# Optimization experiments

Measured on AMD Instinct MI355X. Metric: run time of the kernel, lower is better.

## Reference

```python
import jax, jax.numpy as jnp
import numpy as np

D_MODEL = 4096
D_FF = 11008

def setup_inputs() -> dict:
    key = jax.random.key(0)
    k1, k2, k3, k4 = jax.random.split(key, 4)
    x = jax.random.normal(k1, (2, 2048, D_MODEL), dtype=jnp.float32)
    # Linear weights stored torch-style as [out_features, in_features]
    W_gate = jax.random.normal(k2, (D_FF, D_MODEL), dtype=jnp.float32) * (D_MODEL ** -0.5)
    W_up = jax.random.normal(k3, (D_FF, D_MODEL), dtype=jnp.float32) * (D_MODEL ** -0.5)
    W_down = jax.random.normal(k4, (D_MODEL, D_FF), dtype=jnp.float32) * (D_FF ** -0.5)
    return {"x": x, "W_gate": W_gate, "W_up": W_up, "W_down": W_down}

def reference(x, W_gate, W_up, W_down):
    out_shape = x.shape[:-1] + (W_down.shape[0],)
    xf = x.reshape(-1, x.shape[-1])                      # [T, d_model]
    up = jnp.einsum('td,fd->tf', xf, W_up)               # [T, d_ff]
    gate = jax.nn.silu(jnp.einsum('td,fd->tf', xf, W_gate))  # fused SiLU on gate proj
    h = gate * up                                        # [T, d_ff]
    y = jnp.einsum('tf,df->td', h, W_down)               # [T, d_model]
    return y.reshape(out_shape)
```

## Files before the change

kernel.cpp:

```cpp
#include <hip/hip_runtime.h>
#include <hip/hip_bf16.h>

#define D_MODEL 4096
#define D_FF    11008
#define NTOK    4096

typedef __attribute__((ext_vector_type(8))) short short8;
typedef __attribute__((ext_vector_type(4))) float f32x4;

__global__ void k_cvt(const float* __restrict__ in, __hip_bfloat16* __restrict__ out, int n8) {
    int i = blockIdx.x * blockDim.x + threadIdx.x;
    if (i >= n8) return;
    const float4* p = (const float4*)in;
    float4 v0 = p[(size_t)i * 2];
    float4 v1 = p[(size_t)i * 2 + 1];
    float vals[8] = {v0.x, v0.y, v0.z, v0.w, v1.x, v1.y, v1.z, v1.w};
    short8 o;
#pragma unroll
    for (int j = 0; j < 8; ++j) {
        __hip_bfloat16 b = __float2bfloat16(vals[j]);
        o[j] = *reinterpret_cast<short*>(&b);
    }
    *reinterpret_cast<short8*>(out + (size_t)i * 8) = o;
}

static __device__ __forceinline__ void stage_half(
    const __hip_bfloat16* g, int ld, __hip_bfloat16* lds, int tid)
{
#pragma unroll
    for (int s = 0; s < 2; ++s) {
        int ci = s * 512 + tid;
        int r  = ci >> 3;
        int c  = (ci & 7) ^ (r & 7);
        __builtin_amdgcn_global_load_lds(
            (const __attribute__((address_space(1))) void*)(g + (long)r * ld + c * 8),
            (__attribute__((address_space(3))) void*)(lds + ci * 8),
            16, 0, 0);
    }
}
static __device__ __forceinline__ int sw_off(int row, int kb) {
    return row * 64 + ((((kb >> 3) ^ (row & 7))) << 3);
}

#define MFMA16(a, b, c) __builtin_amdgcn_mfma_f32_16x16x32_bf16(a, b, c, 0, 0, 0)
#define VM4D do { if (pf) asm volatile("s_waitcnt vmcnt(4)" ::: "memory");     \
                  else    asm volatile("s_waitcnt vmcnt(0)" ::: "memory"); } while (0)

#define FPHASE(cA, cB, IQ, LOADB, STAGE, VMC)                                  \
    {                                                                          \
        short8 af[2][2];                                                       \
        _Pragma("unroll")                                                      \
        for (int ii = 0; ii < 2; ++ii)                                         \
            _Pragma("unroll")                                                  \
            for (int kk = 0; kk < 2; ++kk)                                     \
                af[ii][kk] = *reinterpret_cast<const short8*>(                 \
                    &(cA)[sw_off(wm * 128 + ((IQ) * 2 + ii) * 16 + r16,        \
                                 kk * 32 + g4 * 8)]);                          \
        if (LOADB) {                                                           \
            _Pragma("unroll")                                                  \
            for (int kk = 0; kk < 2; ++kk)                                     \
                _Pragma("unroll")                                              \
                for (int j = 0; j < 2; ++j) {                                  \
                    bg[kk][j] = *reinterpret_cast<const short8*>(              \
                        &(cB)[sw_off(wn * 32 + j * 16 + r16,                   \
                                     kk * 32 + g4 * 8)]);                      \
                    bu[kk][j] = *reinterpret_cast<const short8*>(              \
                        &(cB)[8192 + sw_off(wn * 32 + j * 16 + r16,            \
                                            kk * 32 + g4 * 8)]);               \
                }                                                              \
        }                                                                      \
        STAGE;                                                                 \
        VMC;                                                                   \
        if (LOADB) asm volatile("s_waitcnt lgkmcnt(8)" ::: "memory");          \
        __builtin_amdgcn_s_barrier();                                          \
        asm volatile("s_waitcnt lgkmcnt(0)" ::: "memory");                     \
        __builtin_amdgcn_sched_barrier(0);                                     \
        __builtin_amdgcn_s_setprio(1);                                         \
        _Pragma("unroll")                                                      \
        for (int ii = 0; ii < 2; ++ii)                                         \
            _Pragma("unroll")                                                  \
            for (int j = 0; j < 2; ++j) {                                      \
                accg[(IQ) * 2 + ii][j] = MFMA16(af[ii][0], bg[0][j],           \
                                                accg[(IQ) * 2 + ii][j]);       \
                accg[(IQ) * 2 + ii][j] = MFMA16(af[ii][1], bg[1][j],           \
                                                accg[(IQ) * 2 + ii][j]);       \
                accu[(IQ) * 2 + ii][j] = MFMA16(af[ii][0], bu[0][j],           \
                                                accu[(IQ) * 2 + ii][j]);       \
                accu[(IQ) * 2 + ii][j] = MFMA16(af[ii][1], bu[1][j],           \
                                                accu[(IQ) * 2 + ii][j]);       \
            }                                                                  \
        __builtin_amdgcn_s_setprio(0);                                         \
        __builtin_amdgcn_sched_barrier(0);                                     \
        __builtin_amdgcn_s_barrier();                                          \
    }

__global__ __launch_bounds__(512, 2)
void k_gateup(const __hip_bfloat16* __restrict__ X,
              const __hip_bfloat16* __restrict__ Wg,
              const __hip_bfloat16* __restrict__ Wu,
              __hip_bfloat16* __restrict__ H,
              const float* __restrict__ Wd32,
              __hip_bfloat16* __restrict__ Wdb)
{
    extern __shared__ __hip_bfloat16 smem[];
    __hip_bfloat16* sA = smem;
    __hip_bfloat16* sB = smem + 32768;

    const int tid = threadIdx.x;
    const int bid = blockIdx.x;

    if (bid >= 1376) {
        const long total8 = (long)D_MODEL * D_FF / 8;
        const long stride = 160L * 512;
        for (long i = (long)(bid - 1376) * 512 + tid; i < total8; i += stride) {
            const float4* p = (const float4*)(Wd32 + i * 8);
            float4 v0 = p[0], v1 = p[1];
            float vals[8] = {v0.x, v0.y, v0.z, v0.w, v1.x, v1.y, v1.z, v1.w};
            short8 oo;
#pragma unroll
            for (int j = 0; j < 8; ++j) {
                __hip_bfloat16 b = __float2bfloat16(vals[j]);
                oo[j] = *reinterpret_cast<short*>(&b);
            }
            *reinterpret_cast<short8*>(Wdb + i * 8) = oo;
        }
        return;
    }

    const int lane = tid & 63;
    const int wid  = tid >> 6;
    const int wm = wid >> 2, wn = wid & 3;
    const int r16 = lane & 15, g4 = lane >> 4;

    const int xcd = bid & 7;
    const int o   = bid >> 3;
    const int n0 = (o >> 1) * 128;
    const int m0 = (xcd * 2 + (o & 1)) * 256;

    const int K = D_MODEL;
    const __hip_bfloat16* Ab = X  + (long)m0 * K;
    const __hip_bfloat16* Gb = Wg + (long)n0 * K;
    const __hip_bfloat16* Ub = Wu + (long)n0 * K;
    const long h1 = (long)128 * K;

    stage_half(Ab,        K, sA + 0,             tid);
    stage_half(Ab + h1,   K, sA + 8192,          tid);
    stage_half(Gb,        K, sB + 0,             tid);
    stage_half(Ub,        K, sB + 8192,          tid);
    stage_half(Gb + 64,   K, sB + 16384,         tid);
    stage_half(Ub + 64,   K, sB + 16384 + 8192,  tid);
    asm volatile("s_waitcnt vmcnt(4)" ::: "memory");
    __builtin_amdgcn_s_barrier();

    f32x4 accg[8][2], accu[8][2];
#pragma unroll
    for (int i = 0; i < 8; ++i)
#pragma unroll
        for (int j = 0; j < 2; ++j) {
            accg[i][j] = (f32x4){0.f, 0.f, 0.f, 0.f};
            accu[i][j] = (f32x4){0.f, 0.f, 0.f, 0.f};
        }

    const int nk = D_MODEL >> 6;
    const int niter = nk >> 1;

    for (int it = 0; it < niter; ++it) {
        const bool pf = (it + 1 < niter);
        const long ko  = (long)(2 * it + 1) * 64;
        const long kn2 = (long)(2 * it + 2) * 64;
        const long kn3 = (long)(2 * it + 3) * 64;
        short8 bg[2][2], bu[2][2];
        {
            const __hip_bfloat16* cA = sA;
            const __hip_bfloat16* cB = sB;
            FPHASE(cA, cB, 0, 1,
                stage_half(Ab + ko,      K, sA + 16384,        tid), );
            FPHASE(cA, cB, 1, 0,
                stage_half(Ab + h1 + ko, K, sA + 16384 + 8192, tid), );
            FPHASE(cA, cB, 2, 0,
                if (pf) stage_half(Gb + kn2, K, sB + 0,    tid), );
            FPHASE(cA, cB, 3, 0,
                if (pf) stage_half(Ub + kn2, K, sB + 8192, tid), VM4D);
        }
        {
            const __hip_bfloat16* cA = sA + 16384;
            const __hip_bfloat16* cB = sB + 16384;
            FPHASE(cA, cB, 0, 1,
                if (pf) stage_half(Ab + kn2,      K, sA + 0,    tid), );
            FPHASE(cA, cB, 1, 0,
                if (pf) stage_half(Ab + h1 + kn2, K, sA + 8192, tid), );
            FPHASE(cA, cB, 2, 0,
                if (pf) stage_half(Gb + kn3, K, sB + 16384,        tid), );
            FPHASE(cA, cB, 3, 0,
                if (pf) stage_half(Ub + kn3, K, sB + 16384 + 8192, tid), VM4D);
        }
    }

#pragma unroll
    for (int i = 0; i < 8; ++i)
#pragma unroll
        for (int j = 0; j < 2; ++j)
#pragma unroll
            for (int r = 0; r < 4; ++r) {
                long row = m0 + wm * 128 + i * 16 + g4 * 4 + r;
                long col = n0 + wn * 32 + j * 16 + r16;
                float g = accg[i][j][r];
                float u = accu[i][j][r];
                float s = g / (1.f + __expf(-g));
                H[row * D_FF + col] = __float2bfloat16(s * u);
            }
}

#define DPHASE(cA, cB, IQ, LOADB, STAGE, VMC)                                  \
    {                                                                          \
        short8 af[2][2];                                                       \
        _Pragma("unroll")                                                      \
        for (int ii = 0; ii < 2; ++ii)                                         \
            _Pragma("unroll")                                                  \
            for (int kk = 0; kk < 2; ++kk)                                     \
                af[ii][kk] = *reinterpret_cast<const short8*>(                 \
                    &(cA)[sw_off(wm * 128 + ((IQ) * 2 + ii) * 16 + r16,        \
                                 kk * 32 + g4 * 8)]);                          \
        if (LOADB) {                                                           \
            _Pragma("unroll")                                                  \
            for (int kk = 0; kk < 2; ++kk)                                     \
                _Pragma("unroll")                                              \
                for (int j = 0; j < 4; ++j)                                    \
                    bfr[kk][j] = *reinterpret_cast<const short8*>(             \
                        &(cB)[sw_off(wn * 64 + j * 16 + r16,                   \
                                     kk * 32 + g4 * 8)]);                      \
        }                                                                      \
        STAGE;                                                                 \
        VMC;                                                                   \
        if (LOADB) asm volatile("s_waitcnt lgkmcnt(8)" ::: "memory");          \
        __builtin_amdgcn_s_barrier();                                          \
        asm volatile("s_waitcnt lgkmcnt(0)" ::: "memory");                     \
        __builtin_amdgcn_sched_barrier(0);                                     \
        __builtin_amdgcn_s_setprio(1);                                         \
        _Pragma("unroll")                                                      \
        for (int ii = 0; ii < 2; ++ii)                                         \
            _Pragma("unroll")                                                  \
            for (int j = 0; j < 4; ++j) {                                      \
                acc[(IQ) * 2 + ii][j] = MFMA16(af[ii][0], bfr[0][j],           \
                                               acc[(IQ) * 2 + ii][j]);         \
                acc[(IQ) * 2 + ii][j] = MFMA16(af[ii][1], bfr[1][j],           \
                                               acc[(IQ) * 2 + ii][j]);         \
            }                                                                  \
        __builtin_amdgcn_s_setprio(0);                                         \
        __builtin_amdgcn_sched_barrier(0);                                     \
        __builtin_amdgcn_s_barrier();                                          \
    }

__global__ __launch_bounds__(512, 2)
void k_down(const __hip_bfloat16* __restrict__ A,
            const __hip_bfloat16* __restrict__ B,
            float* __restrict__ Y)
{
    extern __shared__ __hip_bfloat16 smem[];
    __hip_bfloat16* sA = smem;
    __hip_bfloat16* sB = smem + 32768;

    const int tid  = threadIdx.x;
    const int lane = tid & 63;
    const int wid  = tid >> 6;
    const int wm = wid >> 2, wn = wid & 3;
    const int r16 = lane & 15, g4 = lane >> 4;

    const int bid = blockIdx.x;
    const int o = (bid & 7) * 32 + (bid >> 3);
    const int n0 = (o >> 4) << 8;
    const int m0 = (o & 15) << 8;

    const int K = D_FF;
    const int N = D_MODEL;
    const __hip_bfloat16* Ab = A + (long)m0 * K;
    const __hip_bfloat16* Bb = B + (long)n0 * K;
    const long h1 = (long)128 * K;

    stage_half(Ab,            K, sA + 0,             tid);
    stage_half(Ab + h1,       K, sA + 8192,          tid);
    stage_half(Bb,            K, sB + 0,             tid);
    stage_half(Bb + h1,       K, sB + 8192,          tid);
    stage_half(Bb + 64,       K, sB + 16384,         tid);
    stage_half(Bb + h1 + 64,  K, sB + 16384 + 8192,  tid);
    asm volatile("s_waitcnt vmcnt(4)" ::: "memory");
    __builtin_amdgcn_s_barrier();

    f32x4 acc[8][4];
#pragma unroll
    for (int i = 0; i < 8; ++i)
#pragma unroll
        for (int j = 0; j < 4; ++j)
            acc[i][j] = (f32x4){0.f, 0.f, 0.f, 0.f};

    const int nk = K >> 6;
    const int niter = nk >> 1;

    for (int it = 0; it < niter; ++it) {
        const bool pf = (it + 1 < niter);
        const long ko  = (long)(2 * it + 1) * 64;
        const long kn2 = (long)(2 * it + 2) * 64;
        const long kn3 = (long)(2 * it + 3) * 64;
        {
            const __hip_bfloat16* cA = sA;
            const __hip_bfloat16* cB = sB;
            short8 bfr[2][4];
            DPHASE(cA, cB, 0, 1,
                stage_half(Ab + ko,      K, sA + 16384,        tid), );
            DPHASE(cA, cB, 1, 0,
                stage_half(Ab + h1 + ko, K, sA + 16384 + 8192, tid), );
            DPHASE(cA, cB, 2, 0,
                if (pf) stage_half(Bb + kn2,      K, sB + 0,    tid), );
            DPHASE(cA, cB, 3, 0,
                if (pf) stage_half(Bb + h1 + kn2, K, sB + 8192, tid), VM4D);
        }
        {
            const __hip_bfloat16* cA = sA + 16384;
            const __hip_bfloat16* cB = sB + 16384;
            short8 bfr[2][4];
            DPHASE(cA, cB, 0, 1,
                if (pf) stage_half(Ab + kn2,      K, sA + 0,    tid), );
            DPHASE(cA, cB, 1, 0,
                if (pf) stage_half(Ab + h1 + kn2, K, sA + 8192, tid), );
            DPHASE(cA, cB, 2, 0,
                if (pf) stage_half(Bb + kn3,      K, sB + 16384, tid), );
            DPHASE(cA, cB, 3, 0,
                if (pf) stage_half(Bb + h1 + kn3, K, sB + 16384 + 8192, tid), VM4D);
        }
    }

#pragma unroll
    for (int i = 0; i < 8; ++i)
#pragma unroll
        for (int j = 0; j < 4; ++j)
#pragma unroll
            for (int r = 0; r < 4; ++r) {
                long row = m0 + wm * 128 + i * 16 + g4 * 4 + r;
                long col = n0 + wn * 64 + j * 16 + r16;
                Y[row * N + col] = acc[i][j][r];
            }
}

extern "C" void kernel_launch(void* const* d_in, const int* in_sizes, int n_in,
                              void* d_out, int out_size, void* d_ws, size_t ws_size,
                              hipStream_t stream) {
    const float* x  = (const float*)d_in[0];
    const float* wg = (const float*)d_in[1];
    const float* wu = (const float*)d_in[2];
    const float* wd = (const float*)d_in[3];
    float* y = (float*)d_out;

    char* ws = (char*)d_ws;
    const size_t szX = (size_t)NTOK * D_MODEL * 2;
    const size_t szW = (size_t)D_FF * D_MODEL * 2;
    __hip_bfloat16* Xb  = (__hip_bfloat16*)(ws);
    __hip_bfloat16* Wgb = (__hip_bfloat16*)(ws + szX);
    __hip_bfloat16* Wub = (__hip_bfloat16*)(ws + szX + szW);
    __hip_bfloat16* Wdb = (__hip_bfloat16*)(ws + szX + 2 * szW);
    __hip_bfloat16* Hb  = (__hip_bfloat16*)(ws + szX + 3 * szW);
    (void)ws_size; (void)out_size; (void)n_in; (void)in_sizes;

    const int SMEM = 131072;
    hipFuncSetAttribute((const void*)k_gateup, hipFuncAttributeMaxDynamicSharedMemorySize, SMEM);
    hipFuncSetAttribute((const void*)k_down,   hipFuncAttributeMaxDynamicSharedMemorySize, SMEM);

    const int nX = NTOK * D_MODEL / 8;
    const int nW = D_FF * D_MODEL / 8;
    k_cvt<<<(nX + 255) / 256, 256, 0, stream>>>(x, Xb, nX);
    k_cvt<<<(nW + 255) / 256, 256, 0, stream>>>(wg, Wgb, nW);
    k_cvt<<<(nW + 255) / 256, 256, 0, stream>>>(wu, Wub, nW);

    k_gateup<<<1536, 512, SMEM, stream>>>(Xb, Wgb, Wub, Hb, wd, Wdb);
    k_down<<<256, 512, SMEM, stream>>>(Hb, Wdb, y);
}
```

Baseline: 1.004 ms.

## Fuse fp32-to-bf16 weight conversion into gate/up GEMM staging

Drops the two separate conversion kernels for W_gate and W_up. The gate/up GEMM now loads fp32 weights into registers, converts them to bf16 and writes them to LDS inside the pipelined main loop, and the block-to-tile mapping is reworked. This removes the extra write and read of the bf16 weight copies. In exchange each block re-reads fp32 weights (twice the bytes per tile, repeated across the 16 M-tiles), uses more registers, and adds a synchronous register-to-LDS path in place of the asynchronous global_load_lds.

```diff
diff --git a/kernel.cpp b/kernel.cpp
--- a/kernel.cpp
+++ b/kernel.cpp
@@ -42,7 +42,34 @@
     return row * 64 + ((((kb >> 3) ^ (row & 7))) << 3);
 }
 
+#define LOADW32(w0, w1, src)                                                   \
+    _Pragma("unroll")                                                          \
+    for (int s = 0; s < 2; ++s) {                                              \
+        int ci = s * 512 + tid;                                                \
+        int rr = ci >> 3, cc = (ci & 7) ^ (rr & 7);                            \
+        const f32x4* gp = reinterpret_cast<const f32x4*>(                      \
+            (src) + (long)rr * 4096 + cc * 8);                                 \
+        w0[s] = gp[0]; w1[s] = gp[1];                                          \
+    }
+
+#define WRITEW32(w0, w1, ldsbase)                                              \
+    _Pragma("unroll")                                                          \
+    for (int s = 0; s < 2; ++s) {                                              \
+        int ci = s * 512 + tid;                                                \
+        short8 pk;                                                             \
+        _Pragma("unroll")                                                      \
+        for (int e = 0; e < 4; ++e) {                                          \
+            __hip_bfloat16 b0 = __float2bfloat16(w0[s][e]);                    \
+            __hip_bfloat16 b1 = __float2bfloat16(w1[s][e]);                    \
+            pk[e]     = *reinterpret_cast<short*>(&b0);                        \
+            pk[4 + e] = *reinterpret_cast<short*>(&b1);                        \
+        }                                                                      \
+        *reinterpret_cast<short8*>((ldsbase) + ci * 8) = pk;                   \
+    }
+
 #define MFMA16(a, b, c) __builtin_amdgcn_mfma_f32_16x16x32_bf16(a, b, c, 0, 0, 0)
+#define VM8 asm volatile("s_waitcnt vmcnt(8)" ::: "memory")
+#define VM0 asm volatile("s_waitcnt vmcnt(0)" ::: "memory")
 #define VM4D do { if (pf) asm volatile("s_waitcnt vmcnt(4)" ::: "memory");     \
                   else    asm volatile("s_waitcnt vmcnt(0)" ::: "memory"); } while (0)
 
@@ -94,10 +121,29 @@
         __builtin_amdgcn_s_barrier();                                          \
     }
 
+#define GUTILE(XB, PF1, PF2, kA, kW)                                           \
+    {                                                                          \
+        const __hip_bfloat16* cA = sA + (XB) * 16384;                          \
+        const __hip_bfloat16* cB = sB + (XB) * 16384;                          \
+        __hip_bfloat16* nA = sA + ((XB) ^ 1) * 16384;                          \
+        __hip_bfloat16* wB = sB + (XB) * 16384;                                \
+        FPHASE(cA, cB, 0, 1,                                                   \
+            if (PF1) { stage_half(Ab + (kA),      4096, nA,        tid);       \
+                       stage_half(Ab + h1 + (kA), 4096, nA + 8192, tid); }, ); \
+        FPHASE(cA, cB, 1, 0,                                                   \
+            if (PF2) { LOADW32(wg0, wg1, G32 + (kW))                           \
+                       LOADW32(wu0, wu1, U32 + (kW)) }, );                     \
+        FPHASE(cA, cB, 2, 0, , VM8);                                           \
+        FPHASE(cA, cB, 3, 0,                                                   \
+            { VM0;                                                             \
+              if (PF2) { WRITEW32(wg0, wg1, wB)                                \
+                         WRITEW32(wu0, wu1, wB + 8192) } }, );                 \
+    }
+
 __global__ __launch_bounds__(512, 2)
 void k_gateup(const __hip_bfloat16* __restrict__ X,
-              const __hip_bfloat16* __restrict__ Wg,
-              const __hip_bfloat16* __restrict__ Wu,
+              const float* __restrict__ Wg,
+              const float* __restrict__ Wu,
               __hip_bfloat16* __restrict__ H,
               const float* __restrict__ Wd32,
               __hip_bfloat16* __restrict__ Wdb)
@@ -132,24 +178,30 @@
     const int wm = wid >> 2, wn = wid & 3;
     const int r16 = lane & 15, g4 = lane >> 4;
 
-    const int xcd = bid & 7;
-    const int o   = bid >> 3;
-    const int n0 = (o >> 1) * 128;
-    const int m0 = (xcd * 2 + (o & 1)) * 256;
-
-    const int K = D_MODEL;
-    const __hip_bfloat16* Ab = X  + (long)m0 * K;
-    const __hip_bfloat16* Gb = Wg + (long)n0 * K;
-    const __hip_bfloat16* Ub = Wu + (long)n0 * K;
-    const long h1 = (long)128 * K;
-
-    stage_half(Ab,        K, sA + 0,             tid);
-    stage_half(Ab + h1,   K, sA + 8192,          tid);
-    stage_half(Gb,        K, sB + 0,             tid);
-    stage_half(Ub,        K, sB + 8192,          tid);
-    stage_half(Gb + 64,   K, sB + 16384,         tid);
-    stage_half(Ub + 64,   K, sB + 16384 + 8192,  tid);
-    asm volatile("s_waitcnt vmcnt(4)" ::: "memory");
+    const int o = (bid & 7) * 172 + (bid >> 3);
+    const int n0 = (o >> 4) * 128;
+    const int m0 = (o & 15) * 256;
+
+    const __hip_bfloat16* Ab = X + (long)m0 * 4096;
+    const float* G32 = Wg + (long)n0 * 4096;
+    const float* U32 = Wu + (long)n0 * 4096;
+    const long h1 = (long)128 * 4096;
+
+    f32x4 wg0[2], wg1[2], wu0[2], wu1[2];
+
+    stage_half(Ab,      4096, sA + 0,    tid);
+    stage_half(Ab + h1, 4096, sA + 8192, tid);
+    LOADW32(wg0, wg1, G32)
+    LOADW32(wu0, wu1, U32)
+    VM0;
+    WRITEW32(wg0, wg1, sB)
+    WRITEW32(wu0, wu1, sB + 8192)
+    LOADW32(wg0, wg1, G32 + 64)
+    LOADW32(wu0, wu1, U32 + 64)
+    VM0;
+    WRITEW32(wg0, wg1, sB + 16384)
+    WRITEW32(wu0, wu1, sB + 16384 + 8192)
+    asm volatile("s_waitcnt lgkmcnt(0)" ::: "memory");
     __builtin_amdgcn_s_barrier();
 
     f32x4 accg[8][2], accu[8][2];
@@ -162,38 +214,16 @@
         }
 
     const int nk = D_MODEL >> 6;
-    const int niter = nk >> 1;
-
-    for (int it = 0; it < niter; ++it) {
-        const bool pf = (it + 1 < niter);
-        const long ko  = (long)(2 * it + 1) * 64;
-        const long kn2 = (long)(2 * it + 2) * 64;
-        const long kn3 = (long)(2 * it + 3) * 64;
-        short8 bg[2][2], bu[2][2];
-        {
-            const __hip_bfloat16* cA = sA;
-            const __hip_bfloat16* cB = sB;
-            FPHASE(cA, cB, 0, 1,
-                stage_half(Ab + ko,      K, sA + 16384,        tid), );
-            FPHASE(cA, cB, 1, 0,
-                stage_half(Ab + h1 + ko, K, sA + 16384 + 8192, tid), );
-            FPHASE(cA, cB, 2, 0,
-                if (pf) stage_half(Gb + kn2, K, sB + 0,    tid), );
-            FPHASE(cA, cB, 3, 0,
-                if (pf) stage_half(Ub + kn2, K, sB + 8192, tid), VM4D);
-        }
-        {
-            const __hip_bfloat16* cA = sA + 16384;
-            const __hip_bfloat16* cB = sB + 16384;
-            FPHASE(cA, cB, 0, 1,
-                if (pf) stage_half(Ab + kn2,      K, sA + 0,    tid), );
-            FPHASE(cA, cB, 1, 0,
-                if (pf) stage_half(Ab + h1 + kn2, K, sA + 8192, tid), );
-            FPHASE(cA, cB, 2, 0,
-                if (pf) stage_half(Gb + kn3, K, sB + 16384,        tid), );
-            FPHASE(cA, cB, 3, 0,
-                if (pf) stage_half(Ub + kn3, K, sB + 16384 + 8192, tid), VM4D);
-        }
+    short8 bg[2][2], bu[2][2];
+
+    for (int it = 0; it < (nk >> 1); ++it) {
+        const int t0 = 2 * it, t1 = 2 * it + 1;
+        const bool p1a = (t0 + 1 < nk), p2a = (t0 + 2 < nk);
+        const bool p1b = (t1 + 1 < nk), p2b = (t1 + 2 < nk);
+        const long kA0 = (long)(t0 + 1) * 64, kW0 = (long)(t0 + 2) * 64;
+        const long kA1 = (long)(t1 + 1) * 64, kW1 = (long)(t1 + 2) * 64;
+        GUTILE(0, p1a, p2a, kA0, kW0)
+        GUTILE(1, p1b, p2b, kA1, kW1)
     }
 
 #pragma unroll
@@ -351,13 +381,11 @@
     float* y = (float*)d_out;
 
     char* ws = (char*)d_ws;
-    const size_t szX = (size_t)NTOK * D_MODEL * 2;
-    const size_t szW = (size_t)D_FF * D_MODEL * 2;
+    const size_t szX  = (size_t)NTOK * D_MODEL * 2;
+    const size_t szWd = (size_t)D_MODEL * D_FF * 2;
     __hip_bfloat16* Xb  = (__hip_bfloat16*)(ws);
-    __hip_bfloat16* Wgb = (__hip_bfloat16*)(ws + szX);
-    __hip_bfloat16* Wub = (__hip_bfloat16*)(ws + szX + szW);
-    __hip_bfloat16* Wdb = (__hip_bfloat16*)(ws + szX + 2 * szW);
-    __hip_bfloat16* Hb  = (__hip_bfloat16*)(ws + szX + 3 * szW);
+    __hip_bfloat16* Wdb = (__hip_bfloat16*)(ws + szX);
+    __hip_bfloat16* Hb  = (__hip_bfloat16*)(ws + szX + szWd);
     (void)ws_size; (void)out_size; (void)n_in; (void)in_sizes;
 
     const int SMEM = 131072;
@@ -365,11 +393,8 @@
     hipFuncSetAttribute((const void*)k_down,   hipFuncAttributeMaxDynamicSharedMemorySize, SMEM);
 
     const int nX = NTOK * D_MODEL / 8;
-    const int nW = D_FF * D_MODEL / 8;
     k_cvt<<<(nX + 255) / 256, 256, 0, stream>>>(x, Xb, nX);
-    k_cvt<<<(nW + 255) / 256, 256, 0, stream>>>(wg, Wgb, nW);
-    k_cvt<<<(nW + 255) / 256, 256, 0, stream>>>(wu, Wub, nW);
-
-    k_gateup<<<1536, 512, SMEM, stream>>>(Xb, Wgb, Wub, Hb, wd, Wdb);
+
+    k_gateup<<<1536, 512, SMEM, stream>>>(Xb, wg, wu, Hb, wd, Wdb);
     k_down<<<256, 512, SMEM, stream>>>(Hb, Wdb, y);
 }
```

Result: slower. 1.206 ms (+20.1%).

## Triple-buffer activation tiles in gate/up GEMM and remap blocks per XCD

Applied to the files above, without the earlier changes.

The gate/up kernel now keeps three LDS stages for the X tile instead of two. The loop becomes a fully unrolled rotation of buffer indices, and two k-steps are prefetched in the prologue. This is meant to give global loads more time to land before the MFMA phases need them. The block-to-tile mapping also changes so that each XCD processes a contiguous range of weight columns across all token tiles, which is meant to improve L2 reuse of the weight tiles. The cost is LDS growing to 160KB per block, which leaves no room for a second resident block, and the X tiles are now read by every XCD.

```diff
diff --git a/kernel.cpp b/kernel.cpp
--- a/kernel.cpp
+++ b/kernel.cpp
@@ -43,6 +43,8 @@
 }
 
 #define MFMA16(a, b, c) __builtin_amdgcn_mfma_f32_16x16x32_bf16(a, b, c, 0, 0, 0)
+#define VM4  asm volatile("s_waitcnt vmcnt(4)" ::: "memory")
+#define VM0A asm volatile("s_waitcnt vmcnt(0)" ::: "memory")
 #define VM4D do { if (pf) asm volatile("s_waitcnt vmcnt(4)" ::: "memory");     \
                   else    asm volatile("s_waitcnt vmcnt(0)" ::: "memory"); } while (0)
 
@@ -94,6 +96,33 @@
         __builtin_amdgcn_s_barrier();                                          \
     }
 
+#define GUGROUP(IT, CS0, CS1, WS0, WS1, PF, VML)                               \
+    {                                                                          \
+        const long kA2 = (long)(2 * (IT) + 2) * 64;                            \
+        const long kA3 = kA2 + 64;                                             \
+        const __hip_bfloat16* cA0 = sA + (CS0) * 16384;                        \
+        const __hip_bfloat16* cA1 = sA + (CS1) * 16384;                        \
+        __hip_bfloat16* w0 = sA + (WS0) * 16384;                               \
+        __hip_bfloat16* w1 = sA + (WS1) * 16384;                               \
+        short8 bg[2][2], bu[2][2];                                             \
+        FPHASE(cA0, sB, 0, 1,                                                  \
+            if (PF) stage_half(Ab + kA2,      4096, w0,        tid), );        \
+        FPHASE(cA0, sB, 1, 0,                                                  \
+            if (PF) stage_half(Ab + h1 + kA2, 4096, w0 + 8192, tid), );        \
+        FPHASE(cA0, sB, 2, 0,                                                  \
+            if (PF) stage_half(Gb + kA2, 4096, sB,        tid), );             \
+        FPHASE(cA0, sB, 3, 0,                                                  \
+            if (PF) stage_half(Ub + kA2, 4096, sB + 8192, tid), VML);          \
+        FPHASE(cA1, sB + 16384, 0, 1,                                          \
+            if (PF) stage_half(Ab + kA3,      4096, w1,        tid), );        \
+        FPHASE(cA1, sB + 16384, 1, 0,                                          \
+            if (PF) stage_half(Ab + h1 + kA3, 4096, w1 + 8192, tid), );        \
+        FPHASE(cA1, sB + 16384, 2, 0,                                          \
+            if (PF) stage_half(Gb + kA3, 4096, sB + 16384,        tid), );     \
+        FPHASE(cA1, sB + 16384, 3, 0,                                          \
+            if (PF) stage_half(Ub + kA3, 4096, sB + 16384 + 8192, tid), VML);  \
+    }
+
 __global__ __launch_bounds__(512, 2)
 void k_gateup(const __hip_bfloat16* __restrict__ X,
               const __hip_bfloat16* __restrict__ Wg,
@@ -104,7 +133,7 @@
 {
     extern __shared__ __hip_bfloat16 smem[];
     __hip_bfloat16* sA = smem;
-    __hip_bfloat16* sB = smem + 32768;
+    __hip_bfloat16* sB = smem + 49152;
 
     const int tid = threadIdx.x;
     const int bid = blockIdx.x;
@@ -132,24 +161,24 @@
     const int wm = wid >> 2, wn = wid & 3;
     const int r16 = lane & 15, g4 = lane >> 4;
 
-    const int xcd = bid & 7;
-    const int o   = bid >> 3;
-    const int n0 = (o >> 1) * 128;
-    const int m0 = (xcd * 2 + (o & 1)) * 256;
-
-    const int K = D_MODEL;
-    const __hip_bfloat16* Ab = X  + (long)m0 * K;
-    const __hip_bfloat16* Gb = Wg + (long)n0 * K;
-    const __hip_bfloat16* Ub = Wu + (long)n0 * K;
-    const long h1 = (long)128 * K;
-
-    stage_half(Ab,        K, sA + 0,             tid);
-    stage_half(Ab + h1,   K, sA + 8192,          tid);
-    stage_half(Gb,        K, sB + 0,             tid);
-    stage_half(Ub,        K, sB + 8192,          tid);
-    stage_half(Gb + 64,   K, sB + 16384,         tid);
-    stage_half(Ub + 64,   K, sB + 16384 + 8192,  tid);
-    asm volatile("s_waitcnt vmcnt(4)" ::: "memory");
+    const int o = (bid & 7) * 172 + (bid >> 3);
+    const int n0 = (o >> 4) * 128;
+    const int m0 = (o & 15) * 256;
+
+    const __hip_bfloat16* Ab = X  + (long)m0 * 4096;
+    const __hip_bfloat16* Gb = Wg + (long)n0 * 4096;
+    const __hip_bfloat16* Ub = Wu + (long)n0 * 4096;
+    const long h1 = (long)128 * 4096;
+
+    stage_half(Ab,           4096, sA + 0,              tid);
+    stage_half(Ab + h1,      4096, sA + 8192,           tid);
+    stage_half(Gb,           4096, sB + 0,              tid);
+    stage_half(Ub,           4096, sB + 8192,           tid);
+    stage_half(Ab + 64,      4096, sA + 16384,          tid);
+    stage_half(Ab + h1 + 64, 4096, sA + 16384 + 8192,   tid);
+    stage_half(Gb + 64,      4096, sB + 16384,          tid);
+    stage_half(Ub + 64,      4096, sB + 16384 + 8192,   tid);
+    asm volatile("s_waitcnt vmcnt(8)" ::: "memory");
     __builtin_amdgcn_s_barrier();
 
     f32x4 accg[8][2], accu[8][2];
@@ -161,40 +190,14 @@
             accu[i][j] = (f32x4){0.f, 0.f, 0.f, 0.f};
         }
 
-    const int nk = D_MODEL >> 6;
-    const int niter = nk >> 1;
-
-    for (int it = 0; it < niter; ++it) {
-        const bool pf = (it + 1 < niter);
-        const long ko  = (long)(2 * it + 1) * 64;
-        const long kn2 = (long)(2 * it + 2) * 64;
-        const long kn3 = (long)(2 * it + 3) * 64;
-        short8 bg[2][2], bu[2][2];
-        {
-            const __hip_bfloat16* cA = sA;
-            const __hip_bfloat16* cB = sB;
-            FPHASE(cA, cB, 0, 1,
-                stage_half(Ab + ko,      K, sA + 16384,        tid), );
-            FPHASE(cA, cB, 1, 0,
-                stage_half(Ab + h1 + ko, K, sA + 16384 + 8192, tid), );
-            FPHASE(cA, cB, 2, 0,
-                if (pf) stage_half(Gb + kn2, K, sB + 0,    tid), );
-            FPHASE(cA, cB, 3, 0,
-                if (pf) stage_half(Ub + kn2, K, sB + 8192, tid), VM4D);
-        }
-        {
-            const __hip_bfloat16* cA = sA + 16384;
-            const __hip_bfloat16* cB = sB + 16384;
-            FPHASE(cA, cB, 0, 1,
-                if (pf) stage_half(Ab + kn2,      K, sA + 0,    tid), );
-            FPHASE(cA, cB, 1, 0,
-                if (pf) stage_half(Ab + h1 + kn2, K, sA + 8192, tid), );
-            FPHASE(cA, cB, 2, 0,
-                if (pf) stage_half(Gb + kn3, K, sB + 16384,        tid), );
-            FPHASE(cA, cB, 3, 0,
-                if (pf) stage_half(Ub + kn3, K, sB + 16384 + 8192, tid), VM4D);
-        }
-    }
+    for (int j = 0; j < 10; ++j) {
+        const int it = 3 * j;
+        GUGROUP(it,     0, 1, 2, 0, true, VM4)
+        GUGROUP(it + 1, 2, 0, 1, 2, true, VM4)
+        GUGROUP(it + 2, 1, 2, 0, 1, true, VM4)
+    }
+    GUGROUP(30, 0, 1, 2, 0, true,  VM4)
+    GUGROUP(31, 2, 0, 1, 2, false, VM0A)
 
 #pragma unroll
     for (int i = 0; i < 8; ++i)
@@ -360,9 +363,10 @@
     __hip_bfloat16* Hb  = (__hip_bfloat16*)(ws + szX + 3 * szW);
     (void)ws_size; (void)out_size; (void)n_in; (void)in_sizes;
 
-    const int SMEM = 131072;
-    hipFuncSetAttribute((const void*)k_gateup, hipFuncAttributeMaxDynamicSharedMemorySize, SMEM);
-    hipFuncSetAttribute((const void*)k_down,   hipFuncAttributeMaxDynamicSharedMemorySize, SMEM);
+    const int SMEM_GU = 163840;
+    const int SMEM_D  = 131072;
+    hipFuncSetAttribute((const void*)k_gateup, hipFuncAttributeMaxDynamicSharedMemorySize, SMEM_GU);
+    hipFuncSetAttribute((const void*)k_down,   hipFuncAttributeMaxDynamicSharedMemorySize, SMEM_D);
 
     const int nX = NTOK * D_MODEL / 8;
     const int nW = D_FF * D_MODEL / 8;
@@ -370,6 +374,6 @@
     k_cvt<<<(nW + 255) / 256, 256, 0, stream>>>(wg, Wgb, nW);
     k_cvt<<<(nW + 255) / 256, 256, 0, stream>>>(wu, Wub, nW);
 
-    k_gateup<<<1536, 512, SMEM, stream>>>(Xb, Wgb, Wub, Hb, wd, Wdb);
-    k_down<<<256, 512, SMEM, stream>>>(Hb, Wdb, y);
-}
+    k_gateup<<<1536, 512, SMEM_GU, stream>>>(Xb, Wgb, Wub, Hb, wd, Wdb);
+    k_down<<<256, 512, SMEM_D, stream>>>(Hb, Wdb, y);
+}
```

Result: no change. 1.019 ms (+1.5%).

## Switch both GEMMs from 16x16x32 to 32x32x16 bf16 MFMA tiles

Applied to the files above, without the earlier changes.

Both the gate/up GEMM and the down GEMM now use 32x32x16 bf16 MFMA instructions instead of 16x16x32, with fragment loads, accumulator layout and epilogue index math rewritten to match. Larger MFMA tiles reuse each LDS fragment across more output elements, which cuts LDS read traffic and instruction count per FLOP. The gate/up block-to-tile mapping also changes to a different XCD-grouped ordering. The 32x32 shape has a different accumulator register layout and a longer per-instruction latency, so register pressure and scheduling may shift.

```diff
diff --git a/kernel.cpp b/kernel.cpp
--- a/kernel.cpp
+++ b/kernel.cpp
@@ -7,6 +7,7 @@
 
 typedef __attribute__((ext_vector_type(8))) short short8;
 typedef __attribute__((ext_vector_type(4))) float f32x4;
+typedef __attribute__((ext_vector_type(16))) float f32x16;
 
 __global__ void k_cvt(const float* __restrict__ in, __hip_bfloat16* __restrict__ out, int n8) {
     int i = blockIdx.x * blockDim.x + threadIdx.x;
@@ -42,32 +43,25 @@
     return row * 64 + ((((kb >> 3) ^ (row & 7))) << 3);
 }
 
-#define MFMA16(a, b, c) __builtin_amdgcn_mfma_f32_16x16x32_bf16(a, b, c, 0, 0, 0)
+#define MFMA32(a, b, c) __builtin_amdgcn_mfma_f32_32x32x16_bf16(a, b, c, 0, 0, 0)
 #define VM4D do { if (pf) asm volatile("s_waitcnt vmcnt(4)" ::: "memory");     \
                   else    asm volatile("s_waitcnt vmcnt(0)" ::: "memory"); } while (0)
 
 #define FPHASE(cA, cB, IQ, LOADB, STAGE, VMC)                                  \
     {                                                                          \
-        short8 af[2][2];                                                       \
+        short8 af[4];                                                          \
         _Pragma("unroll")                                                      \
-        for (int ii = 0; ii < 2; ++ii)                                         \
-            _Pragma("unroll")                                                  \
-            for (int kk = 0; kk < 2; ++kk)                                     \
-                af[ii][kk] = *reinterpret_cast<const short8*>(                 \
-                    &(cA)[sw_off(wm * 128 + ((IQ) * 2 + ii) * 16 + r16,        \
-                                 kk * 32 + g4 * 8)]);                          \
+        for (int ks = 0; ks < 4; ++ks)                                         \
+            af[ks] = *reinterpret_cast<const short8*>(                         \
+                &(cA)[sw_off(wm * 128 + (IQ) * 32 + l31, ks * 16 + hi8)]);     \
         if (LOADB) {                                                           \
             _Pragma("unroll")                                                  \
-            for (int kk = 0; kk < 2; ++kk)                                     \
-                _Pragma("unroll")                                              \
-                for (int j = 0; j < 2; ++j) {                                  \
-                    bg[kk][j] = *reinterpret_cast<const short8*>(              \
-                        &(cB)[sw_off(wn * 32 + j * 16 + r16,                   \
-                                     kk * 32 + g4 * 8)]);                      \
-                    bu[kk][j] = *reinterpret_cast<const short8*>(              \
-                        &(cB)[8192 + sw_off(wn * 32 + j * 16 + r16,            \
-                                            kk * 32 + g4 * 8)]);               \
-                }                                                              \
+            for (int ks = 0; ks < 4; ++ks) {                                   \
+                bg[ks] = *reinterpret_cast<const short8*>(                     \
+                    &(cB)[sw_off(wn * 32 + l31, ks * 16 + hi8)]);              \
+                bu[ks] = *reinterpret_cast<const short8*>(                     \
+                    &(cB)[8192 + sw_off(wn * 32 + l31, ks * 16 + hi8)]);       \
+            }                                                                  \
         }                                                                      \
         STAGE;                                                                 \
         VMC;                                                                   \
@@ -77,18 +71,10 @@
         __builtin_amdgcn_sched_barrier(0);                                     \
         __builtin_amdgcn_s_setprio(1);                                         \
         _Pragma("unroll")                                                      \
-        for (int ii = 0; ii < 2; ++ii)                                         \
-            _Pragma("unroll")                                                  \
-            for (int j = 0; j < 2; ++j) {                                      \
-                accg[(IQ) * 2 + ii][j] = MFMA16(af[ii][0], bg[0][j],           \
-                                                accg[(IQ) * 2 + ii][j]);       \
-                accg[(IQ) * 2 + ii][j] = MFMA16(af[ii][1], bg[1][j],           \
-                                                accg[(IQ) * 2 + ii][j]);       \
-                accu[(IQ) * 2 + ii][j] = MFMA16(af[ii][0], bu[0][j],           \
-                                                accu[(IQ) * 2 + ii][j]);       \
-                accu[(IQ) * 2 + ii][j] = MFMA16(af[ii][1], bu[1][j],           \
-                                                accu[(IQ) * 2 + ii][j]);       \
-            }                                                                  \
+        for (int ks = 0; ks < 4; ++ks) {                                       \
+            accg[(IQ)] = MFMA32(af[ks], bg[ks], accg[(IQ)]);                   \
+            accu[(IQ)] = MFMA32(af[ks], bu[ks], accu[(IQ)]);                   \
+        }                                                                      \
         __builtin_amdgcn_s_setprio(0);                                         \
         __builtin_amdgcn_sched_barrier(0);                                     \
         __builtin_amdgcn_s_barrier();                                          \
@@ -130,12 +116,13 @@
     const int lane = tid & 63;
     const int wid  = tid >> 6;
     const int wm = wid >> 2, wn = wid & 3;
-    const int r16 = lane & 15, g4 = lane >> 4;
-
-    const int xcd = bid & 7;
-    const int o   = bid >> 3;
-    const int n0 = (o >> 1) * 128;
-    const int m0 = (xcd * 2 + (o & 1)) * 256;
+    const int l31 = lane & 31;
+    const int hi  = lane >> 5;
+    const int hi8 = hi * 8;
+
+    const int o = (bid & 7) * 172 + (bid >> 3);
+    const int n0 = (o >> 4) * 128;
+    const int m0 = (o & 15) * 256;
 
     const int K = D_MODEL;
     const __hip_bfloat16* Ab = X  + (long)m0 * K;
@@ -152,13 +139,13 @@
     asm volatile("s_waitcnt vmcnt(4)" ::: "memory");
     __builtin_amdgcn_s_barrier();
 
-    f32x4 accg[8][2], accu[8][2];
-#pragma unroll
-    for (int i = 0; i < 8; ++i)
-#pragma unroll
-        for (int j = 0; j < 2; ++j) {
-            accg[i][j] = (f32x4){0.f, 0.f, 0.f, 0.f};
-            accu[i][j] = (f32x4){0.f, 0.f, 0.f, 0.f};
+    f32x16 accg[4], accu[4];
+#pragma unroll
+    for (int i = 0; i < 4; ++i)
+#pragma unroll
+        for (int r = 0; r < 16; ++r) {
+            accg[i][r] = 0.f;
+            accu[i][r] = 0.f;
         }
 
     const int nk = D_MODEL >> 6;
@@ -169,7 +156,7 @@
         const long ko  = (long)(2 * it + 1) * 64;
         const long kn2 = (long)(2 * it + 2) * 64;
         const long kn3 = (long)(2 * it + 3) * 64;
-        short8 bg[2][2], bu[2][2];
+        short8 bg[4], bu[4];
         {
             const __hip_bfloat16* cA = sA;
             const __hip_bfloat16* cB = sB;
@@ -197,38 +184,32 @@
     }
 
 #pragma unroll
-    for (int i = 0; i < 8; ++i)
-#pragma unroll
-        for (int j = 0; j < 2; ++j)
-#pragma unroll
-            for (int r = 0; r < 4; ++r) {
-                long row = m0 + wm * 128 + i * 16 + g4 * 4 + r;
-                long col = n0 + wn * 32 + j * 16 + r16;
-                float g = accg[i][j][r];
-                float u = accu[i][j][r];
-                float s = g / (1.f + __expf(-g));
-                H[row * D_FF + col] = __float2bfloat16(s * u);
-            }
+    for (int i = 0; i < 4; ++i)
+#pragma unroll
+        for (int r = 0; r < 16; ++r) {
+            long row = m0 + wm * 128 + i * 32 + (r & 3) + 8 * (r >> 2) + 4 * hi;
+            long col = n0 + wn * 32 + l31;
+            float g = accg[i][r];
+            float u = accu[i][r];
+            float s = g / (1.f + __expf(-g));
+            H[row * D_FF + col] = __float2bfloat16(s * u);
+        }
 }
 
 #define DPHASE(cA, cB, IQ, LOADB, STAGE, VMC)                                  \
     {                                                                          \
-        short8 af[2][2];                                                       \
+        short8 af[4];                                                          \
         _Pragma("unroll")                                                      \
-        for (int ii = 0; ii < 2; ++ii)                                         \
-            _Pragma("unroll")                                                  \
-            for (int kk = 0; kk < 2; ++kk)                                     \
-                af[ii][kk] = *reinterpret_cast<const short8*>(                 \
-                    &(cA)[sw_off(wm * 128 + ((IQ) * 2 + ii) * 16 + r16,        \
-                                 kk * 32 + g4 * 8)]);                          \
+        for (int ks = 0; ks < 4; ++ks)                                         \
+            af[ks] = *reinterpret_cast<const short8*>(                         \
+                &(cA)[sw_off(wm * 128 + (IQ) * 32 + l31, ks * 16 + hi8)]);     \
         if (LOADB) {                                                           \
             _Pragma("unroll")                                                  \
-            for (int kk = 0; kk < 2; ++kk)                                     \
+            for (int ks = 0; ks < 4; ++ks)                                     \
                 _Pragma("unroll")                                              \
-                for (int j = 0; j < 4; ++j)                                    \
-                    bfr[kk][j] = *reinterpret_cast<const short8*>(             \
-                        &(cB)[sw_off(wn * 64 + j * 16 + r16,                   \
-                                     kk * 32 + g4 * 8)]);                      \
+                for (int j = 0; j < 2; ++j)                                    \
+                    bfr[ks][j] = *reinterpret_cast<const short8*>(             \
+                        &(cB)[sw_off(wn * 64 + j * 32 + l31, ks * 16 + hi8)]); \
         }                                                                      \
         STAGE;                                                                 \
         VMC;                                                                   \
@@ -238,14 +219,10 @@
         __builtin_amdgcn_sched_barrier(0);                                     \
         __builtin_amdgcn_s_setprio(1);                                         \
         _Pragma("unroll")                                                      \
-        for (int ii = 0; ii < 2; ++ii)                                         \
+        for (int ks = 0; ks < 4; ++ks)                                         \
             _Pragma("unroll")                                                  \
-            for (int j = 0; j < 4; ++j) {                                      \
-                acc[(IQ) * 2 + ii][j] = MFMA16(af[ii][0], bfr[0][j],           \
-                                               acc[(IQ) * 2 + ii][j]);         \
-                acc[(IQ) * 2 + ii][j] = MFMA16(af[ii][1], bfr[1][j],           \
-                                               acc[(IQ) * 2 + ii][j]);         \
-            }                                                                  \
+            for (int j = 0; j < 2; ++j)                                        \
+                acc[(IQ)][j] = MFMA32(af[ks], bfr[ks][j], acc[(IQ)][j]);       \
         __builtin_amdgcn_s_setprio(0);                                         \
         __builtin_amdgcn_sched_barrier(0);                                     \
         __builtin_amdgcn_s_barrier();                                          \
@@ -264,7 +241,9 @@
     const int lane = tid & 63;
     const int wid  = tid >> 6;
     const int wm = wid >> 2, wn = wid & 3;
-    const int r16 = lane & 15, g4 = lane >> 4;
+    const int l31 = lane & 31;
+    const int hi  = lane >> 5;
+    const int hi8 = hi * 8;
 
     const int bid = blockIdx.x;
     const int o = (bid & 7) * 32 + (bid >> 3);
@@ -286,12 +265,14 @@
     asm volatile("s_waitcnt vmcnt(4)" ::: "memory");
     __builtin_amdgcn_s_barrier();
 
-    f32x4 acc[8][4];
-#pragma unroll
-    for (int i = 0; i < 8; ++i)
-#pragma unroll
-        for (int j = 0; j < 4; ++j)
-            acc[i][j] = (f32x4){0.f, 0.f, 0.f, 0.f};
+    f32x16 acc[4][2];
+#pragma unroll
+    for (int i = 0; i < 4; ++i)
+#pragma unroll
+        for (int j = 0; j < 2; ++j)
+#pragma unroll
+            for (int r = 0; r < 16; ++r)
+                acc[i][j][r] = 0.f;
 
     const int nk = K >> 6;
     const int niter = nk >> 1;
@@ -304,7 +285,7 @@
         {
             const __hip_bfloat16* cA = sA;
             const __hip_bfloat16* cB = sB;
-            short8 bfr[2][4];
+            short8 bfr[4][2];
             DPHASE(cA, cB, 0, 1,
                 stage_half(Ab + ko,      K, sA + 16384,        tid), );
             DPHASE(cA, cB, 1, 0,
@@ -317,7 +298,7 @@
         {
             const __hip_bfloat16* cA = sA + 16384;
             const __hip_bfloat16* cB = sB + 16384;
-            short8 bfr[2][4];
+            short8 bfr[4][2];
             DPHASE(cA, cB, 0, 1,
                 if (pf) stage_half(Ab + kn2,      K, sA + 0,    tid), );
             DPHASE(cA, cB, 1, 0,
@@ -330,13 +311,13 @@
     }
 
 #pragma unroll
-    for (int i = 0; i < 8; ++i)
-#pragma unroll
-        for (int j = 0; j < 4; ++j)
-#pragma unroll
-            for (int r = 0; r < 4; ++r) {
-                long row = m0 + wm * 128 + i * 16 + g4 * 4 + r;
-                long col = n0 + wn * 64 + j * 16 + r16;
+    for (int i = 0; i < 4; ++i)
+#pragma unroll
+        for (int j = 0; j < 2; ++j)
+#pragma unroll
+            for (int r = 0; r < 16; ++r) {
+                long row = m0 + wm * 128 + i * 32 + (r & 3) + 8 * (r >> 2) + 4 * hi;
+                long col = n0 + wn * 64 + j * 32 + l31;
                 Y[row * N + col] = acc[i][j][r];
             }
 }
```

New measurement: 1.100 ms. +9.6%, slower.
